# Performance work log

Hardware: AMD Instinct MI355X
Metric: run time of the kernel (lower is better)

Reference implementation:

```python
import jax, jax.numpy as jnp
import numpy as np

DECAY = 0.99


def setup_inputs() -> dict:
    key = jax.random.key(0)
    k1, k2, k3 = jax.random.split(key, 3)
    B, D, H, W = 16, 128, 32, 32
    K = 8192
    z_e = jax.random.normal(k1, (B, D, H, W), dtype=jnp.float32)
    codebook = jax.random.normal(k2, (K, D), dtype=jnp.float32)
    ema_count = jnp.ones((K,), dtype=jnp.float32)
    ema_weight = codebook  # buffer initialized as codebook.clone()
    return {"z_e": z_e, "codebook": codebook, "ema_count": ema_count, "ema_weight": ema_weight}


def reference(z_e, codebook, ema_count, ema_weight):
    B, D, H, W = z_e.shape
    K = codebook.shape[0]
    # (B,D,H,W) -> (N,D)
    z_flat = z_e.transpose(0, 2, 3, 1).reshape(-1, D)
    # squared L2 distances: ||z||^2 - 2 z.C^T + ||C||^2  -> (N,K)
    dist = (
        jnp.sum(z_flat * z_flat, axis=1, keepdims=True)
        - 2.0 * (z_flat @ codebook.T)
        + jnp.sum(codebook * codebook, axis=1)[None, :]
    )
    indices = jnp.argmin(dist, axis=1)  # (N,)
    z_q = codebook[indices].reshape(B, H, W, D).transpose(0, 3, 1, 2)
    # EMA codebook update (training path, no grad)
    counts = jax.ops.segment_sum(jnp.ones_like(indices, dtype=jnp.float32), indices, num_segments=K)
    dw = jax.ops.segment_sum(z_flat, indices, num_segments=K)  # (K,D)
    new_count = ema_count * DECAY + (1.0 - DECAY) * counts
    new_weight = ema_weight * DECAY + (1.0 - DECAY) * dw
    new_codebook = new_weight / jnp.maximum(new_count, 1.0)[:, None]
    # straight-through estimator
    z_q_st = z_e + jax.lax.stop_gradient(z_q - z_e)
    return (z_q_st, indices.reshape(B, H, W), new_codebook, new_count, new_weight)
```

## Files before the change

kernel.cpp:

```cpp
#include <hip/hip_runtime.h>

#define D 128
#define HW 1024
#define NROWS 16384
#define K 8192
#define NU 32

#define OUT0 0
#define OUT1 2097152
#define OUT2 2113536
#define OUT3 3162112
#define OUT4 3170304

typedef __attribute__((ext_vector_type(8))) _Float16 half8;
typedef __attribute__((ext_vector_type(16))) float f32x16;
typedef unsigned short u16;
typedef unsigned long long u64;

__device__ __forceinline__ void gld16(const u16* gsrc, u16* ldst) {
    __builtin_amdgcn_global_load_lds(
        (const __attribute__((address_space(1))) unsigned int*)gsrc,
        (__attribute__((address_space(3))) unsigned int*)ldst,
        16, 0, 0);
}

__global__ __launch_bounds__(256) void k_prep(const float* __restrict__ cb,
                                              const float* __restrict__ z_e,
                                              u16* __restrict__ Bg,
                                              float* __restrict__ cnorm,
                                              u16* __restrict__ Ah, u16* __restrict__ Al,
                                              u64* __restrict__ packed,
                                              float* __restrict__ counts,
                                              float* __restrict__ dw) {
    const int tid = threadIdx.x;
    if (blockIdx.x < 512) {
        int kk = tid & 15;
        int k = blockIdx.x * 16 + (tid >> 4);
        const float* src = cb + (size_t)k * D + kk * 8;
        half8 h, l;
        float s = 0.f;
#pragma unroll
        for (int j = 0; j < 8; ++j) {
            float v = src[j];
            s += v * v;
            _Float16 hv = (_Float16)v;
            _Float16 lv = (_Float16)(v - (float)hv);
            h[j] = hv;
            l[j] = lv;
        }
        int g = k >> 6, col = k & 63;
        size_t offH = (size_t)g * 16384 + ((size_t)kk * 64 + col) * 8;
        *(half8*)((_Float16*)Bg + offH) = h;
        *(half8*)((_Float16*)Bg + offH + 8192) = l;
#pragma unroll
        for (int off = 8; off > 0; off >>= 1) s += __shfl_down(s, off);
        if (kk == 0) cnorm[k] = s;
        float4 z4 = {0.f, 0.f, 0.f, 0.f};
        size_t zi = ((size_t)blockIdx.x * 256 + tid) * 8;
        *(float4*)(dw + zi) = z4;
        *(float4*)(dw + zi + 4) = z4;
    } else {
        int gid = (blockIdx.x - 512) * 256 + tid;
        int n  = gid & (NROWS - 1);
        int kk = gid >> 14;
        int b = n >> 10, hw = n & 1023;
        const float* src = z_e + ((size_t)b * D + kk * 8) * HW + hw;
        half8 h, l;
#pragma unroll
        for (int j = 0; j < 8; ++j) {
            float v = src[(size_t)j * HW];
            _Float16 hv = (_Float16)v;
            _Float16 lv = (_Float16)(v - (float)hv);
            h[j] = hv;
            l[j] = lv;
        }
        int rg = n >> 7, band = (n >> 5) & 3, row = n & 31;
        size_t off = (((((size_t)rg * 4 + band) * 8 + (kk >> 1)) * 2 + (kk & 1)) * 32 + row) * 8;
        *(half8*)(Ah + off) = h;
        *(half8*)(Al + off) = l;
        if (kk == 0) {
            packed[n] = ~0ull;
            if (n < K) counts[n] = 0.f;
        }
    }
}

__global__ __launch_bounds__(512, 4) void k_argmin_mfma(
        const u16* __restrict__ Ahg, const u16* __restrict__ Alg,
        const u16* __restrict__ Bg,
        const float* __restrict__ cnorm, u64* __restrict__ packed) {
    __shared__ u16 lds[2][16384];

    const int tid = threadIdx.x;
    const int ln  = tid & 63;
    const int l31 = ln & 31;
    const int lh  = ln >> 5;
    const int wv  = tid >> 6;
    const int wy  = wv & 3;
    const int wx  = wv >> 2;

    const int rg = blockIdx.x >> 2;
    const int k0 = (blockIdx.x & 3) * 2048;
    const int g0 = k0 >> 6;

    half8 Ah[8], Al[8];
#pragma unroll
    for (int ks = 0; ks < 8; ++ks) {
        size_t off = ((((size_t)(rg * 4 + wy) * 8 + ks) * 2 + lh) * 32 + l31) * 8;
        Ah[ks] = *(const half8*)((const _Float16*)Ahg + off);
        Al[ks] = *(const half8*)((const _Float16*)Alg + off);
    }

    {
        const u16* src = Bg + (size_t)g0 * 16384;
#pragma unroll
        for (int r = 0; r < 4; ++r)
            gld16(src + ((size_t)r * 512 + tid) * 8, lds[0] + (r * 512 + tid) * 8);
    }

    float minv[16];
    int   mini[16];
#pragma unroll
    for (int r = 0; r < 16; ++r) { minv[r] = INFINITY; mini[r] = 0; }

#pragma unroll 1
    for (int u = 0; u < NU; ++u) {
        const u16* buf = lds[u & 1];
        const int c0 = k0 + u * 64 + wx * 32 + l31;

        float cn0 = cnorm[c0];

        if (u + 1 < NU) {
            const u16* src = Bg + (size_t)(g0 + u + 1) * 16384;
            u16* dst = lds[(u + 1) & 1];
#pragma unroll
            for (int r = 0; r < 4; ++r)
                gld16(src + ((size_t)r * 512 + tid) * 8, dst + (r * 512 + tid) * 8);
            asm volatile("s_waitcnt vmcnt(4)" ::: "memory");
        } else {
            asm volatile("s_waitcnt vmcnt(0)" ::: "memory");
        }
        asm volatile("s_barrier" ::: "memory");

        f32x16 acc = {};
        const _Float16* bh = (const _Float16*)buf;
        const _Float16* bl = bh + 8192;

#pragma unroll
        for (int ks = 0; ks < 8; ++ks) {
            const int bo = ((ks * 2 + lh) * 64 + wx * 32 + l31) * 8;
            half8 b0 = *(const half8*)(bl + bo);
            acc = __builtin_amdgcn_mfma_f32_32x32x16_f16(Ah[ks], b0, acc, 0, 0, 0);
        }
#pragma unroll
        for (int ks = 0; ks < 8; ++ks) {
            const int bo = ((ks * 2 + lh) * 64 + wx * 32 + l31) * 8;
            half8 b0 = *(const half8*)(bh + bo);
            acc = __builtin_amdgcn_mfma_f32_32x32x16_f16(Ah[ks], b0, acc, 0, 0, 0);
            acc = __builtin_amdgcn_mfma_f32_32x32x16_f16(Al[ks], b0, acc, 0, 0, 0);
        }

#pragma unroll
        for (int r = 0; r < 16; ++r) {
            float d0 = fmaf(-2.0f, acc[r], cn0);
            if (d0 < minv[r]) { minv[r] = d0; mini[r] = c0; }
        }
        asm volatile("s_barrier" ::: "memory");
    }

#pragma unroll
    for (int r = 0; r < 16; ++r) {
        float v = minv[r];
        int ix = mini[r];
#pragma unroll
        for (int off = 1; off < 32; off <<= 1) {
            float v2 = __shfl_xor(v, off);
            int i2 = __shfl_xor(ix, off);
            if (v2 < v || (v2 == v && i2 < ix)) { v = v2; ix = i2; }
        }
        if (l31 == 0) {
            int row = rg * 128 + wy * 32 + 4 * lh + (r & 3) + 8 * (r >> 2);
            unsigned int uenc = __float_as_uint(v);
            uenc = (uenc & 0x80000000u) ? ~uenc : (uenc | 0x80000000u);
            u64 pk = ((u64)uenc << 13) | (u64)(unsigned)ix;
            atomicMin(&packed[row], pk);
        }
    }
}

__global__ __launch_bounds__(256) void k_epilogue(const float* __restrict__ z_e,
                                                  const float* __restrict__ cb,
                                                  const u64* __restrict__ packed,
                                                  float* __restrict__ out0,
                                                  float* __restrict__ out1,
                                                  float* __restrict__ counts,
                                                  float* __restrict__ dw) {
    __shared__ int idxS[64];
    const int tid = threadIdx.x;
    const int n0 = blockIdx.x * 64;
    const int bb = n0 >> 10, p0 = n0 & 1023;

    if (tid < 64) {
        int ix = (int)(packed[n0 + tid] & 0x1FFFull);
        idxS[tid] = ix;
        out1[n0 + tid] = (float)ix;
        atomicAdd(&counts[ix], 1.0f);
    }
    __syncthreads();

    const float* zb = z_e + (size_t)bb * (D * HW) + p0;
    float* ob = out0 + (size_t)bb * (D * HW) + p0;

    for (int i = tid; i < 64 * D; i += 256) {
        int d = i >> 6, r = i & 63;
        float z = zb[(size_t)d * HW + r];
        float c = cb[(size_t)idxS[r] * D + d];
        ob[(size_t)d * HW + r] = z + (c - z);
    }
    for (int i = tid; i < 64 * D; i += 256) {
        int r = i >> 7, d = i & 127;
        atomicAdd(&dw[(size_t)idxS[r] * D + d], zb[(size_t)d * HW + r]);
    }
}

__global__ __launch_bounds__(256) void k_final(const float* __restrict__ ema_count,
                                               const float* __restrict__ ema_weight,
                                               float* __restrict__ out2,
                                               float* __restrict__ out3,
                                               float* __restrict__ out4) {
    int gid = blockIdx.x * 256 + threadIdx.x;
    int k = gid >> 7, d = gid & 127;
    float cnt_raw = out3[k];
    float dw_raw = out4[gid];
    __syncthreads();
    float nc = 0.99f * ema_count[k] + 0.01f * cnt_raw;
    float nw = 0.99f * ema_weight[gid] + 0.01f * dw_raw;
    out4[gid] = nw;
    out2[gid] = nw / fmaxf(nc, 1.0f);
    if (d == 0) out3[k] = nc;
}

extern "C" void kernel_launch(void* const* d_in, const int* in_sizes, int n_in,
                              void* d_out, int out_size, void* d_ws, size_t ws_size,
                              hipStream_t stream) {
    const float* z_e        = (const float*)d_in[0];
    const float* cb         = (const float*)d_in[1];
    const float* ema_count  = (const float*)d_in[2];
    const float* ema_weight = (const float*)d_in[3];
    float* out = (float*)d_out;

    float* cnorm = (float*)d_ws;
    u64* packed = (u64*)((char*)d_ws + K * 4);

    u16* Ahg = (u16*)(out + OUT0);
    u16* Alg = Ahg + (size_t)NROWS * D;
    u16* Bg  = (u16*)(out + OUT2);

    k_prep       <<<1536,          256, 0, stream>>>(cb, z_e, Bg, cnorm, Ahg, Alg,
                                                     packed, out + OUT3, out + OUT4);
    k_argmin_mfma<<<512,           512, 0, stream>>>(Ahg, Alg, Bg, cnorm, packed);
    k_epilogue   <<<NROWS / 64,    256, 0, stream>>>(z_e, cb, packed,
                                                     out + OUT0, out + OUT1,
                                                     out + OUT3, out + OUT4);
    k_final      <<<(K * D) / 256, 256, 0, stream>>>(ema_count, ema_weight,
                                                     out + OUT2, out + OUT3, out + OUT4);
}
```

Measured before the change: 205.6 us.

## Fuse z_e fp16 split into argmin kernel and shrink tiles to 64 rows

Drops the separate pass that converts z_e into a hi/lo fp16 layout. Each argmin wave now loads its z_e rows directly and splits them in registers. The argmin block shrinks to 256 threads covering 64 rows, and the grid doubles to 1024 blocks. The codebook staging is split into K-halves, so each LDS buffer is half the size, with twice as many barriers per column group. This saves the global write and re-read of the A operand and the prep work. In exchange, z_e is read with strided, uncoalesced loads inside the hot kernel, and codebook tiles are reloaded twice as often across row groups.

```diff
diff --git a/kernel.cpp b/kernel.cpp
--- a/kernel.cpp
+++ b/kernel.cpp
@@ -4,7 +4,6 @@
 #define HW 1024
 #define NROWS 16384
 #define K 8192
-#define NU 32
 
 #define OUT0 0
 #define OUT1 2097152
@@ -24,98 +23,82 @@
         16, 0, 0);
 }
 
-__global__ __launch_bounds__(256) void k_prep(const float* __restrict__ cb,
-                                              const float* __restrict__ z_e,
-                                              u16* __restrict__ Bg,
-                                              float* __restrict__ cnorm,
-                                              u16* __restrict__ Ah, u16* __restrict__ Al,
-                                              u64* __restrict__ packed,
-                                              float* __restrict__ counts,
-                                              float* __restrict__ dw) {
+__global__ __launch_bounds__(256) void k_prep_cb(const float* __restrict__ cb,
+                                                 u16* __restrict__ Bg,
+                                                 float* __restrict__ cnorm,
+                                                 u64* __restrict__ packed,
+                                                 float* __restrict__ counts,
+                                                 float* __restrict__ dw) {
     const int tid = threadIdx.x;
-    if (blockIdx.x < 512) {
-        int kk = tid & 15;
-        int k = blockIdx.x * 16 + (tid >> 4);
-        const float* src = cb + (size_t)k * D + kk * 8;
+    int kk = tid & 15;
+    int k = blockIdx.x * 16 + (tid >> 4);
+    const float* src = cb + (size_t)k * D + kk * 8;
+    half8 h, l;
+    float s = 0.f;
+#pragma unroll
+    for (int j = 0; j < 8; ++j) {
+        float v = src[j];
+        s += v * v;
+        _Float16 hv = (_Float16)v;
+        _Float16 lv = (_Float16)(v - (float)hv);
+        h[j] = hv;
+        l[j] = lv;
+    }
+    int g = k >> 6, col = k & 63, khalf = kk >> 3, kq = kk & 7;
+    size_t base = ((size_t)(g * 2 + khalf)) * 8192 + ((size_t)kq * 64 + col) * 8;
+    *(half8*)((_Float16*)Bg + base) = h;
+    *(half8*)((_Float16*)Bg + base + 4096) = l;
+#pragma unroll
+    for (int off = 8; off > 0; off >>= 1) s += __shfl_down(s, off);
+    if (kk == 0) cnorm[k] = s;
+    float4 z4 = {0.f, 0.f, 0.f, 0.f};
+    size_t zi = ((size_t)blockIdx.x * 256 + tid) * 8;
+    *(float4*)(dw + zi) = z4;
+    *(float4*)(dw + zi + 4) = z4;
+    if (blockIdx.x < 64) packed[blockIdx.x * 256 + tid] = ~0ull;
+    else if (blockIdx.x < 96) counts[(blockIdx.x - 64) * 256 + tid] = 0.f;
+}
+
+__global__ __launch_bounds__(256, 4) void k_argmin_mfma(
+        const float* __restrict__ z_e,
+        const u16* __restrict__ Bg,
+        const float* __restrict__ cnorm, u64* __restrict__ packed) {
+    __shared__ u16 lds[2][8192];
+
+    const int tid = threadIdx.x;
+    const int ln  = tid & 63;
+    const int l31 = ln & 31;
+    const int lh  = ln >> 5;
+    const int wy  = (tid >> 6) & 1;
+    const int wx  = tid >> 7;
+
+    const int rg = blockIdx.x >> 2;
+    const int k0 = (blockIdx.x & 3) * 2048;
+    const int s0 = (k0 >> 6) * 2;
+
+    const int rowA = rg * 64 + wy * 32 + l31;
+    const float* za = z_e + (size_t)(rowA >> 10) * (D * HW) + (rowA & 1023);
+    half8 Ah[8], Al[8];
+#pragma unroll
+    for (int ks = 0; ks < 8; ++ks) {
         half8 h, l;
-        float s = 0.f;
 #pragma unroll
         for (int j = 0; j < 8; ++j) {
-            float v = src[j];
-            s += v * v;
+            float v = za[(size_t)(ks * 16 + lh * 8 + j) * HW];
             _Float16 hv = (_Float16)v;
             _Float16 lv = (_Float16)(v - (float)hv);
             h[j] = hv;
             l[j] = lv;
         }
-        int g = k >> 6, col = k & 63;
-        size_t offH = (size_t)g * 16384 + ((size_t)kk * 64 + col) * 8;
-        *(half8*)((_Float16*)Bg + offH) = h;
-        *(half8*)((_Float16*)Bg + offH + 8192) = l;
-#pragma unroll
-        for (int off = 8; off > 0; off >>= 1) s += __shfl_down(s, off);
-        if (kk == 0) cnorm[k] = s;
-        float4 z4 = {0.f, 0.f, 0.f, 0.f};
-        size_t zi = ((size_t)blockIdx.x * 256 + tid) * 8;
-        *(float4*)(dw + zi) = z4;
-        *(float4*)(dw + zi + 4) = z4;
-    } else {
-        int gid = (blockIdx.x - 512) * 256 + tid;
-        int n  = gid & (NROWS - 1);
-        int kk = gid >> 14;
-        int b = n >> 10, hw = n & 1023;
-        const float* src = z_e + ((size_t)b * D + kk * 8) * HW + hw;
-        half8 h, l;
-#pragma unroll
-        for (int j = 0; j < 8; ++j) {
-            float v = src[(size_t)j * HW];
-            _Float16 hv = (_Float16)v;
-            _Float16 lv = (_Float16)(v - (float)hv);
-            h[j] = hv;
-            l[j] = lv;
-        }
-        int rg = n >> 7, band = (n >> 5) & 3, row = n & 31;
-        size_t off = (((((size_t)rg * 4 + band) * 8 + (kk >> 1)) * 2 + (kk & 1)) * 32 + row) * 8;
-        *(half8*)(Ah + off) = h;
-        *(half8*)(Al + off) = l;
-        if (kk == 0) {
-            packed[n] = ~0ull;
-            if (n < K) counts[n] = 0.f;
-        }
-    }
-}
-
-__global__ __launch_bounds__(512, 4) void k_argmin_mfma(
-        const u16* __restrict__ Ahg, const u16* __restrict__ Alg,
-        const u16* __restrict__ Bg,
-        const float* __restrict__ cnorm, u64* __restrict__ packed) {
-    __shared__ u16 lds[2][16384];
-
-    const int tid = threadIdx.x;
-    const int ln  = tid & 63;
-    const int l31 = ln & 31;
-    const int lh  = ln >> 5;
-    const int wv  = tid >> 6;
-    const int wy  = wv & 3;
-    const int wx  = wv >> 2;
-
-    const int rg = blockIdx.x >> 2;
-    const int k0 = (blockIdx.x & 3) * 2048;
-    const int g0 = k0 >> 6;
-
-    half8 Ah[8], Al[8];
-#pragma unroll
-    for (int ks = 0; ks < 8; ++ks) {
-        size_t off = ((((size_t)(rg * 4 + wy) * 8 + ks) * 2 + lh) * 32 + l31) * 8;
-        Ah[ks] = *(const half8*)((const _Float16*)Ahg + off);
-        Al[ks] = *(const half8*)((const _Float16*)Alg + off);
+        Ah[ks] = h;
+        Al[ks] = l;
     }
 
     {
-        const u16* src = Bg + (size_t)g0 * 16384;
+        const u16* src = Bg + (size_t)s0 * 8192;
 #pragma unroll
         for (int r = 0; r < 4; ++r)
-            gld16(src + ((size_t)r * 512 + tid) * 8, lds[0] + (r * 512 + tid) * 8);
+            gld16(src + (r * 256 + tid) * 8, lds[0] + (r * 256 + tid) * 8);
     }
 
     float minv[16];
@@ -123,49 +106,46 @@
 #pragma unroll
     for (int r = 0; r < 16; ++r) { minv[r] = INFINITY; mini[r] = 0; }
 
+    const int bo_base = wx * 32 + l31;
+
 #pragma unroll 1
-    for (int u = 0; u < NU; ++u) {
-        const u16* buf = lds[u & 1];
-        const int c0 = k0 + u * 64 + wx * 32 + l31;
-
-        float cn0 = cnorm[c0];
-
-        if (u + 1 < NU) {
-            const u16* src = Bg + (size_t)(g0 + u + 1) * 16384;
-            u16* dst = lds[(u + 1) & 1];
-#pragma unroll
-            for (int r = 0; r < 4; ++r)
-                gld16(src + ((size_t)r * 512 + tid) * 8, dst + (r * 512 + tid) * 8);
-            asm volatile("s_waitcnt vmcnt(4)" ::: "memory");
-        } else {
-            asm volatile("s_waitcnt vmcnt(0)" ::: "memory");
-        }
-        asm volatile("s_barrier" ::: "memory");
-
+    for (int g = 0; g < 32; ++g) {
+        const int colv = k0 + g * 64 + wx * 32 + l31;
+        float cn0 = cnorm[colv];
         f32x16 acc = {};
-        const _Float16* bh = (const _Float16*)buf;
-        const _Float16* bl = bh + 8192;
-
-#pragma unroll
-        for (int ks = 0; ks < 8; ++ks) {
-            const int bo = ((ks * 2 + lh) * 64 + wx * 32 + l31) * 8;
-            half8 b0 = *(const half8*)(bl + bo);
-            acc = __builtin_amdgcn_mfma_f32_32x32x16_f16(Ah[ks], b0, acc, 0, 0, 0);
-        }
-#pragma unroll
-        for (int ks = 0; ks < 8; ++ks) {
-            const int bo = ((ks * 2 + lh) * 64 + wx * 32 + l31) * 8;
-            half8 b0 = *(const half8*)(bh + bo);
-            acc = __builtin_amdgcn_mfma_f32_32x32x16_f16(Ah[ks], b0, acc, 0, 0, 0);
-            acc = __builtin_amdgcn_mfma_f32_32x32x16_f16(Al[ks], b0, acc, 0, 0, 0);
-        }
-
+#pragma unroll
+        for (int half = 0; half < 2; ++half) {
+            const int u = g * 2 + half;
+            if (u + 1 < 64) {
+                const u16* src = Bg + (size_t)(s0 + u + 1) * 8192;
+                u16* dst = lds[1 - half];
+#pragma unroll
+                for (int r = 0; r < 4; ++r)
+                    gld16(src + (r * 256 + tid) * 8, dst + (r * 256 + tid) * 8);
+                asm volatile("s_waitcnt vmcnt(4)" ::: "memory");
+            } else {
+                asm volatile("s_waitcnt vmcnt(0)" ::: "memory");
+            }
+            asm volatile("s_barrier" ::: "memory");
+
+            const _Float16* bh = (const _Float16*)lds[half];
+#pragma unroll
+            for (int ks = 0; ks < 4; ++ks) {
+                const int bo = ((ks * 2 + lh) * 64 + bo_base) * 8;
+                half8 bl = *(const half8*)(bh + 4096 + bo);
+                half8 b0 = *(const half8*)(bh + bo);
+                const int ak = half * 4 + ks;
+                acc = __builtin_amdgcn_mfma_f32_32x32x16_f16(Ah[ak], bl, acc, 0, 0, 0);
+                acc = __builtin_amdgcn_mfma_f32_32x32x16_f16(Ah[ak], b0, acc, 0, 0, 0);
+                acc = __builtin_amdgcn_mfma_f32_32x32x16_f16(Al[ak], b0, acc, 0, 0, 0);
+            }
+            asm volatile("s_barrier" ::: "memory");
+        }
 #pragma unroll
         for (int r = 0; r < 16; ++r) {
             float d0 = fmaf(-2.0f, acc[r], cn0);
-            if (d0 < minv[r]) { minv[r] = d0; mini[r] = c0; }
-        }
-        asm volatile("s_barrier" ::: "memory");
+            if (d0 < minv[r]) { minv[r] = d0; mini[r] = colv; }
+        }
     }
 
 #pragma unroll
@@ -179,7 +159,7 @@
             if (v2 < v || (v2 == v && i2 < ix)) { v = v2; ix = i2; }
         }
         if (l31 == 0) {
-            int row = rg * 128 + wy * 32 + 4 * lh + (r & 3) + 8 * (r >> 2);
+            int row = rg * 64 + wy * 32 + 4 * lh + (r & 3) + 8 * (r >> 2);
             unsigned int uenc = __float_as_uint(v);
             uenc = (uenc & 0x80000000u) ? ~uenc : (uenc | 0x80000000u);
             u64 pk = ((u64)uenc << 13) | (u64)(unsigned)ix;
@@ -252,13 +232,11 @@
     float* cnorm = (float*)d_ws;
     u64* packed = (u64*)((char*)d_ws + K * 4);
 
-    u16* Ahg = (u16*)(out + OUT0);
-    u16* Alg = Ahg + (size_t)NROWS * D;
-    u16* Bg  = (u16*)(out + OUT2);
-
-    k_prep       <<<1536,          256, 0, stream>>>(cb, z_e, Bg, cnorm, Ahg, Alg,
-                                                     packed, out + OUT3, out + OUT4);
-    k_argmin_mfma<<<512,           512, 0, stream>>>(Ahg, Alg, Bg, cnorm, packed);
+    u16* Bg = (u16*)(out + OUT2);
+
+    k_prep_cb    <<<K / 16,        256, 0, stream>>>(cb, Bg, cnorm, packed,
+                                                     out + OUT3, out + OUT4);
+    k_argmin_mfma<<<1024,          256, 0, stream>>>(z_e, Bg, cnorm, packed);
     k_epilogue   <<<NROWS / 64,    256, 0, stream>>>(z_e, cb, packed,
                                                      out + OUT0, out + OUT1,
                                                      out + OUT3, out + OUT4);
```

After: 227.2 us. 10.5% more time.

## Fuse z split into argmin kernel and run epilogue in last-arriving block

Applied to the files above, without the earlier changes.

The fp16 hi/lo split of z_e now happens directly in the argmin kernel, which reads z_e straight from global memory, so the staged A buffers and their prep pass are gone. The epilogue (index write, counts, z_q output, dw scatter) is folded into the same kernel: it runs in whichever of the four column blocks per row group arrives last, detected with a done counter. This removes one launch and a global round trip. The cost is uncoalesced strided z_e loads in the prologue, plus a tail that runs in only a quarter of the blocks. Counts also change to integer atomics, and the MFMA loop is interleaved.

```diff
diff --git a/kernel.cpp b/kernel.cpp
--- a/kernel.cpp
+++ b/kernel.cpp
@@ -12,9 +12,15 @@
 #define OUT3 3162112
 #define OUT4 3170304
 
+#define WS_CNORM   0
+#define WS_PACKED  32768
+#define WS_CNT     163840
+#define WS_DONE    196608
+
 typedef __attribute__((ext_vector_type(8))) _Float16 half8;
 typedef __attribute__((ext_vector_type(16))) float f32x16;
 typedef unsigned short u16;
+typedef unsigned int u32;
 typedef unsigned long long u64;
 
 __device__ __forceinline__ void gld16(const u16* gsrc, u16* ldst) {
@@ -25,71 +31,52 @@
 }
 
 __global__ __launch_bounds__(256) void k_prep(const float* __restrict__ cb,
-                                              const float* __restrict__ z_e,
                                               u16* __restrict__ Bg,
                                               float* __restrict__ cnorm,
-                                              u16* __restrict__ Ah, u16* __restrict__ Al,
                                               u64* __restrict__ packed,
-                                              float* __restrict__ counts,
+                                              u32* __restrict__ cnt,
+                                              u32* __restrict__ done,
                                               float* __restrict__ dw) {
     const int tid = threadIdx.x;
-    if (blockIdx.x < 512) {
-        int kk = tid & 15;
-        int k = blockIdx.x * 16 + (tid >> 4);
-        const float* src = cb + (size_t)k * D + kk * 8;
-        half8 h, l;
-        float s = 0.f;
-#pragma unroll
-        for (int j = 0; j < 8; ++j) {
-            float v = src[j];
-            s += v * v;
-            _Float16 hv = (_Float16)v;
-            _Float16 lv = (_Float16)(v - (float)hv);
-            h[j] = hv;
-            l[j] = lv;
-        }
-        int g = k >> 6, col = k & 63;
-        size_t offH = (size_t)g * 16384 + ((size_t)kk * 64 + col) * 8;
-        *(half8*)((_Float16*)Bg + offH) = h;
-        *(half8*)((_Float16*)Bg + offH + 8192) = l;
-#pragma unroll
-        for (int off = 8; off > 0; off >>= 1) s += __shfl_down(s, off);
-        if (kk == 0) cnorm[k] = s;
-        float4 z4 = {0.f, 0.f, 0.f, 0.f};
-        size_t zi = ((size_t)blockIdx.x * 256 + tid) * 8;
-        *(float4*)(dw + zi) = z4;
-        *(float4*)(dw + zi + 4) = z4;
-    } else {
-        int gid = (blockIdx.x - 512) * 256 + tid;
-        int n  = gid & (NROWS - 1);
-        int kk = gid >> 14;
-        int b = n >> 10, hw = n & 1023;
-        const float* src = z_e + ((size_t)b * D + kk * 8) * HW + hw;
-        half8 h, l;
-#pragma unroll
-        for (int j = 0; j < 8; ++j) {
-            float v = src[(size_t)j * HW];
-            _Float16 hv = (_Float16)v;
-            _Float16 lv = (_Float16)(v - (float)hv);
-            h[j] = hv;
-            l[j] = lv;
-        }
-        int rg = n >> 7, band = (n >> 5) & 3, row = n & 31;
-        size_t off = (((((size_t)rg * 4 + band) * 8 + (kk >> 1)) * 2 + (kk & 1)) * 32 + row) * 8;
-        *(half8*)(Ah + off) = h;
-        *(half8*)(Al + off) = l;
-        if (kk == 0) {
-            packed[n] = ~0ull;
-            if (n < K) counts[n] = 0.f;
-        }
-    }
-}
-
-__global__ __launch_bounds__(512, 4) void k_argmin_mfma(
-        const u16* __restrict__ Ahg, const u16* __restrict__ Alg,
-        const u16* __restrict__ Bg,
-        const float* __restrict__ cnorm, u64* __restrict__ packed) {
+    int kk = tid & 15;
+    int k = blockIdx.x * 16 + (tid >> 4);
+    const float* src = cb + (size_t)k * D + kk * 8;
+    half8 h, l;
+    float s = 0.f;
+#pragma unroll
+    for (int j = 0; j < 8; ++j) {
+        float v = src[j];
+        s += v * v;
+        _Float16 hv = (_Float16)v;
+        _Float16 lv = (_Float16)(v - (float)hv);
+        h[j] = hv;
+        l[j] = lv;
+    }
+    int g = k >> 6, col = k & 63;
+    size_t offH = (size_t)g * 16384 + ((size_t)kk * 64 + col) * 8;
+    *(half8*)((_Float16*)Bg + offH) = h;
+    *(half8*)((_Float16*)Bg + offH + 8192) = l;
+#pragma unroll
+    for (int off = 8; off > 0; off >>= 1) s += __shfl_down(s, off);
+    if (kk == 0) cnorm[k] = s;
+    float4 z4 = {0.f, 0.f, 0.f, 0.f};
+    size_t zi = ((size_t)blockIdx.x * 256 + tid) * 8;
+    *(float4*)(dw + zi) = z4;
+    *(float4*)(dw + zi + 4) = z4;
+    int gid = blockIdx.x * 256 + tid;
+    if (gid < NROWS) packed[gid] = ~0ull;
+    if (gid < K) cnt[gid] = 0u;
+    if (gid < 128) done[gid] = 0u;
+}
+
+__global__ __launch_bounds__(512, 4) void k_argmin_tail(
+        const float* __restrict__ z_e, const float* __restrict__ cb,
+        const u16* __restrict__ Bg, const float* __restrict__ cnorm,
+        u64* __restrict__ packed, float* __restrict__ out0,
+        float* __restrict__ out1, u32* __restrict__ cnt,
+        u32* __restrict__ done, float* __restrict__ dw) {
     __shared__ u16 lds[2][16384];
+    __shared__ u32 winflag;
 
     const int tid = threadIdx.x;
     const int ln  = tid & 63;
@@ -103,12 +90,22 @@
     const int k0 = (blockIdx.x & 3) * 2048;
     const int g0 = k0 >> 6;
 
+    const int rowA = rg * 128 + wy * 32 + l31;
+    const float* za = z_e + (size_t)(rowA >> 10) * (D * HW) + (rowA & 1023);
     half8 Ah[8], Al[8];
 #pragma unroll
     for (int ks = 0; ks < 8; ++ks) {
-        size_t off = ((((size_t)(rg * 4 + wy) * 8 + ks) * 2 + lh) * 32 + l31) * 8;
-        Ah[ks] = *(const half8*)((const _Float16*)Ahg + off);
-        Al[ks] = *(const half8*)((const _Float16*)Alg + off);
+        half8 h, l;
+#pragma unroll
+        for (int j = 0; j < 8; ++j) {
+            float v = za[(size_t)(ks * 16 + lh * 8 + j) * HW];
+            _Float16 hv = (_Float16)v;
+            _Float16 lv = (_Float16)(v - (float)hv);
+            h[j] = hv;
+            l[j] = lv;
+        }
+        Ah[ks] = h;
+        Al[ks] = l;
     }
 
     {
@@ -123,12 +120,12 @@
 #pragma unroll
     for (int r = 0; r < 16; ++r) { minv[r] = INFINITY; mini[r] = 0; }
 
+    const int bo_base = wx * 32 + l31;
+
 #pragma unroll 1
     for (int u = 0; u < NU; ++u) {
-        const u16* buf = lds[u & 1];
-        const int c0 = k0 + u * 64 + wx * 32 + l31;
-
-        float cn0 = cnorm[c0];
+        const int colv = k0 + u * 64 + wx * 32 + l31;
+        float cn0 = cnorm[colv];
 
         if (u + 1 < NU) {
             const u16* src = Bg + (size_t)(g0 + u + 1) * 16384;
@@ -142,28 +139,23 @@
         }
         asm volatile("s_barrier" ::: "memory");
 
+        const _Float16* bh = (const _Float16*)lds[u & 1];
+        const _Float16* bl = bh + 8192;
         f32x16 acc = {};
-        const _Float16* bh = (const _Float16*)buf;
-        const _Float16* bl = bh + 8192;
-
 #pragma unroll
         for (int ks = 0; ks < 8; ++ks) {
-            const int bo = ((ks * 2 + lh) * 64 + wx * 32 + l31) * 8;
-            half8 b0 = *(const half8*)(bl + bo);
-            acc = __builtin_amdgcn_mfma_f32_32x32x16_f16(Ah[ks], b0, acc, 0, 0, 0);
-        }
-#pragma unroll
-        for (int ks = 0; ks < 8; ++ks) {
-            const int bo = ((ks * 2 + lh) * 64 + wx * 32 + l31) * 8;
-            half8 b0 = *(const half8*)(bh + bo);
-            acc = __builtin_amdgcn_mfma_f32_32x32x16_f16(Ah[ks], b0, acc, 0, 0, 0);
-            acc = __builtin_amdgcn_mfma_f32_32x32x16_f16(Al[ks], b0, acc, 0, 0, 0);
+            const int bo = ((ks * 2 + lh) * 64 + bo_base) * 8;
+            half8 vbl = *(const half8*)(bl + bo);
+            half8 vbh = *(const half8*)(bh + bo);
+            acc = __builtin_amdgcn_mfma_f32_32x32x16_f16(Ah[ks], vbl, acc, 0, 0, 0);
+            acc = __builtin_amdgcn_mfma_f32_32x32x16_f16(Ah[ks], vbh, acc, 0, 0, 0);
+            acc = __builtin_amdgcn_mfma_f32_32x32x16_f16(Al[ks], vbh, acc, 0, 0, 0);
         }
 
 #pragma unroll
         for (int r = 0; r < 16; ++r) {
             float d0 = fmaf(-2.0f, acc[r], cn0);
-            if (d0 < minv[r]) { minv[r] = d0; mini[r] = c0; }
+            if (d0 < minv[r]) { minv[r] = d0; mini[r] = colv; }
         }
         asm volatile("s_barrier" ::: "memory");
     }
@@ -186,55 +178,53 @@
             atomicMin(&packed[row], pk);
         }
     }
-}
-
-__global__ __launch_bounds__(256) void k_epilogue(const float* __restrict__ z_e,
-                                                  const float* __restrict__ cb,
-                                                  const u64* __restrict__ packed,
-                                                  float* __restrict__ out0,
-                                                  float* __restrict__ out1,
-                                                  float* __restrict__ counts,
-                                                  float* __restrict__ dw) {
-    __shared__ int idxS[64];
-    const int tid = threadIdx.x;
-    const int n0 = blockIdx.x * 64;
+
+    __threadfence();
+    __syncthreads();
+    if (tid == 0) winflag = atomicAdd(&done[rg], 1u);
+    __syncthreads();
+    if (winflag != 3u) return;
+
+    __threadfence();
+    int* idxS = (int*)&lds[0][0];
+    const int n0 = rg * 128;
     const int bb = n0 >> 10, p0 = n0 & 1023;
 
-    if (tid < 64) {
-        int ix = (int)(packed[n0 + tid] & 0x1FFFull);
+    if (tid < 128) {
+        u64 p = __hip_atomic_load(&packed[n0 + tid], __ATOMIC_RELAXED,
+                                  __HIP_MEMORY_SCOPE_AGENT);
+        int ix = (int)(p & 0x1FFFull);
         idxS[tid] = ix;
         out1[n0 + tid] = (float)ix;
-        atomicAdd(&counts[ix], 1.0f);
+        atomicAdd(&cnt[ix], 1u);
     }
     __syncthreads();
 
     const float* zb = z_e + (size_t)bb * (D * HW) + p0;
     float* ob = out0 + (size_t)bb * (D * HW) + p0;
 
-    for (int i = tid; i < 64 * D; i += 256) {
-        int d = i >> 6, r = i & 63;
+    for (int i = tid; i < 128 * D; i += 512) {
+        int d = i >> 7, r = i & 127;
         float z = zb[(size_t)d * HW + r];
         float c = cb[(size_t)idxS[r] * D + d];
         ob[(size_t)d * HW + r] = z + (c - z);
     }
-    for (int i = tid; i < 64 * D; i += 256) {
+    for (int i = tid; i < 128 * D; i += 512) {
         int r = i >> 7, d = i & 127;
         atomicAdd(&dw[(size_t)idxS[r] * D + d], zb[(size_t)d * HW + r]);
     }
 }
 
-__global__ __launch_bounds__(256) void k_final(const float* __restrict__ ema_count,
+__global__ __launch_bounds__(256) void k_final(const u32* __restrict__ cnt,
+                                               const float* __restrict__ ema_count,
                                                const float* __restrict__ ema_weight,
                                                float* __restrict__ out2,
                                                float* __restrict__ out3,
                                                float* __restrict__ out4) {
     int gid = blockIdx.x * 256 + threadIdx.x;
     int k = gid >> 7, d = gid & 127;
-    float cnt_raw = out3[k];
-    float dw_raw = out4[gid];
-    __syncthreads();
-    float nc = 0.99f * ema_count[k] + 0.01f * cnt_raw;
-    float nw = 0.99f * ema_weight[gid] + 0.01f * dw_raw;
+    float nc = 0.99f * ema_count[k] + 0.01f * (float)cnt[k];
+    float nw = 0.99f * ema_weight[gid] + 0.01f * out4[gid];
     out4[gid] = nw;
     out2[gid] = nw / fmaxf(nc, 1.0f);
     if (d == 0) out3[k] = nc;
@@ -248,20 +238,21 @@
     const float* ema_count  = (const float*)d_in[2];
     const float* ema_weight = (const float*)d_in[3];
     float* out = (float*)d_out;
-
-    float* cnorm = (float*)d_ws;
-    u64* packed = (u64*)((char*)d_ws + K * 4);
-
-    u16* Ahg = (u16*)(out + OUT0);
-    u16* Alg = Ahg + (size_t)NROWS * D;
-    u16* Bg  = (u16*)(out + OUT2);
-
-    k_prep       <<<1536,          256, 0, stream>>>(cb, z_e, Bg, cnorm, Ahg, Alg,
-                                                     packed, out + OUT3, out + OUT4);
-    k_argmin_mfma<<<512,           512, 0, stream>>>(Ahg, Alg, Bg, cnorm, packed);
-    k_epilogue   <<<NROWS / 64,    256, 0, stream>>>(z_e, cb, packed,
-                                                     out + OUT0, out + OUT1,
-                                                     out + OUT3, out + OUT4);
-    k_final      <<<(K * D) / 256, 256, 0, stream>>>(ema_count, ema_weight,
-                                                     out + OUT2, out + OUT3, out + OUT4);
-}
+    char* ws = (char*)d_ws;
+
+    float* cnorm  = (float*)(ws + WS_CNORM);
+    u64*   packed = (u64*)(ws + WS_PACKED);
+    u32*   cnt    = (u32*)(ws + WS_CNT);
+    u32*   done   = (u32*)(ws + WS_DONE);
+
+    u16* Bg = (u16*)(out + OUT2);
+
+    k_prep       <<<K / 16,        256, 0, stream>>>(cb, Bg, cnorm, packed, cnt,
+                                                     done, out + OUT4);
+    k_argmin_tail<<<512,           512, 0, stream>>>(z_e, cb, Bg, cnorm, packed,
+                                                     out + OUT0, out + OUT1, cnt,
+                                                     done, out + OUT4);
+    k_final      <<<(K * D) / 256, 256, 0, stream>>>(cnt, ema_count, ema_weight,
+                                                     out + OUT2, out + OUT3,
+                                                     out + OUT4);
+}
```

Result: slower. 345.2 us (+67.9%).
